# Kernel optimization log

Hardware: AMD Instinct MI355X
Metric: run time of the kernel (lower is better)

Reference implementation:

```python
import jax, jax.numpy as jnp
import numpy as np

MINIMUM_VALUE = -1e9  # C.MINIMUM_VALUE: large negative fill for masked positions


def setup_inputs() -> dict:
    key = jax.random.key(0)
    kq, kv, km, kw = jax.random.split(key, 4)
    B, N, H = 8, 2048, 1024
    query = jax.random.normal(kq, (B, N, H), dtype=jnp.float32)
    value = jax.random.normal(kv, (B, N, H), dtype=jnp.float32)
    mask = jax.random.randint(km, (B, N, N), 0, 2, dtype=jnp.int32)
    W = jax.random.normal(kw, (H, H), dtype=jnp.float32)
    return {"query": query, "value": value, "mask": mask, "W": W}


def reference(query, value, mask, W):
    # intermediate = query @ W           : B x M x H
    # e = relu(intermediate @ value^T)   : B x M x N
    e = jax.nn.relu(jnp.einsum("bmh,hk,bnk->bmn", query, W, value))
    attn_logits = jnp.where(mask > 0, e, MINIMUM_VALUE)
    attn = jax.nn.softmax(attn_logits, axis=-1)
    output = jnp.einsum("bmn,bnh->bmh", attn, value)
    return (output, attn)
```

## Files before the change

### kernel.cpp

```cpp
#include <hip/hip_runtime.h>


typedef _Float16 half8 __attribute__((ext_vector_type(8)));
typedef float f32x4 __attribute__((ext_vector_type(4)));
typedef unsigned short u16;
typedef unsigned int u32;

#define BATCH 8
#define SEQ   2048
#define HID   1024
#define MINV  (-1e9f)

#define AS1 __attribute__((address_space(1)))
#define AS3 __attribute__((address_space(3)))

__device__ __forceinline__ u16 h2u(_Float16 h) { return __builtin_bit_cast(u16, h); }

__device__ __forceinline__ u32 packhl(float x) {
    _Float16 h = (_Float16)x;
    _Float16 l = (_Float16)(x - (float)h);
    return (u32)h2u(h) | ((u32)h2u(l) << 16);
}

__device__ __forceinline__ void gload16(const char* g, AS3 char* l) {
    __builtin_amdgcn_global_load_lds((const AS1 void*)g, (AS3 void*)l, 16, 0, 0);
}

__global__ __launch_bounds__(256) void prep_v(const float* __restrict__ V,
                                              u16* __restrict__ Vp,
                                              u16* __restrict__ Vt)
{
    __shared__ __align__(16) u16 lt[64 * 72];
    const int b = blockIdx.z, n0 = blockIdx.y * 64, h0 = blockIdx.x * 64;
    const int t = threadIdx.x;
    const int r = t >> 4, c4 = (t & 15) * 4;
#pragma unroll
    for (int it = 0; it < 4; ++it) {
        const int rr = r + it * 16;
        const float4 x = *(const float4*)(V + ((size_t)b * SEQ + n0 + rr) * HID + h0 + c4);
        const float xs[4] = {x.x, x.y, x.z, x.w};
        u32 p[4];
#pragma unroll
        for (int e = 0; e < 4; ++e) {
            p[e] = packhl(xs[e]);
            lt[(c4 + e) * 72 + rr] = (u16)p[e];
        }
        const int g = (h0 + c4) >> 5, j = c4 & 31;
        u16* base = Vp + (((size_t)b * SEQ + n0 + rr) * 32 + g) * 64;
        *(uint2*)(base + j) = make_uint2((p[0] & 0xffffu) | (p[1] << 16),
                                         (p[2] & 0xffffu) | (p[3] << 16));
        *(uint2*)(base + 32 + j) = make_uint2((p[0] >> 16) | (p[1] & 0xffff0000u),
                                              (p[2] >> 16) | (p[3] & 0xffff0000u));
    }
    __syncthreads();
    const int hr = t >> 2, cc = (t & 3) * 2;
    uint4 v0 = *(const uint4*)&lt[hr * 72 + cc * 8];
    uint4 v1 = *(const uint4*)&lt[hr * 72 + cc * 8 + 8];
    u16* dst = Vt + ((size_t)b * HID + h0 + hr) * SEQ + n0 + cc * 8;
    *(uint4*)dst = v0;
    *(uint4*)(dst + 8) = v1;
}

__global__ __launch_bounds__(256) void prep_w(const float* __restrict__ W,
                                              u16* __restrict__ Wtp)
{
    __shared__ __align__(16) u32 lt[64 * 68];
    const int n0 = blockIdx.x * 64, k0 = blockIdx.y * 64;
    const int t = threadIdx.x;
    const int r = t >> 4, c4 = (t & 15) * 4;
#pragma unroll
    for (int it = 0; it < 4; ++it) {
        const int rr = r + it * 16;
        const float4 x = *(const float4*)(W + (size_t)(k0 + rr) * HID + n0 + c4);
        const float xs[4] = {x.x, x.y, x.z, x.w};
#pragma unroll
        for (int e = 0; e < 4; ++e) lt[(c4 + e) * 68 + rr] = packhl(xs[e]);
    }
    __syncthreads();
    const int n = t >> 2;
#pragma unroll
    for (int s = 0; s < 4; ++s) {
        const int ci = (t & 3) + s * 4;
        uint4 v = *(const uint4*)&lt[n * 68 + ci * 4];
        const int k = k0 + ci * 4;
        u16* base = Wtp + (((size_t)n0 + n) * 32 + (k >> 5)) * 64;
        const int j = k & 31;
        *(uint2*)(base + j) = make_uint2((v.x & 0xffffu) | (v.y << 16),
                                         (v.z & 0xffffu) | (v.w << 16));
        *(uint2*)(base + 32 + j) = make_uint2((v.x >> 16) | (v.y & 0xffff0000u),
                                              (v.z >> 16) | (v.w & 0xffff0000u));
    }
}

__global__ __launch_bounds__(256) void prep_q(const float* __restrict__ Q,
                                              u16* __restrict__ Qp)
{
    const size_t row = blockIdx.x;
    const int t = threadIdx.x;
    const float4 x = ((const float4*)(Q + row * HID))[t];
    const u32 p0 = packhl(x.x), p1 = packhl(x.y), p2 = packhl(x.z), p3 = packhl(x.w);
    const int k = t * 4;
    u16* base = Qp + (row * 32 + (k >> 5)) * 64;
    const int j = k & 31;
    *(uint2*)(base + j) = make_uint2((p0 & 0xffffu) | (p1 << 16),
                                     (p2 & 0xffffu) | (p3 << 16));
    *(uint2*)(base + 32 + j) = make_uint2((p0 >> 16) | (p1 & 0xffff0000u),
                                          (p2 >> 16) | (p3 & 0xffff0000u));
}

template <bool SPLIT>
__device__ __forceinline__ void cluster4x2(f32x4 (&acc)[8][4], int ib, int jb,
                                           const half8 (&ah)[4], const half8 (&al)[4],
                                           half8 bh0, half8 bl0, half8 bh1, half8 bl1)
{
#pragma unroll
    for (int f = 0; f < 4; ++f) {
#pragma unroll
        for (int jj = 0; jj < 2; ++jj) {
            const half8 bh = jj ? bh1 : bh0;
            const half8 bl = jj ? bl1 : bl0;
            f32x4 c = acc[ib + f][jb + jj];
            if constexpr (SPLIT) {
                c = __builtin_amdgcn_mfma_f32_16x16x32_f16(al[f], bh, c, 0, 0, 0);
                c = __builtin_amdgcn_mfma_f32_16x16x32_f16(ah[f], bl, c, 0, 0, 0);
                c = __builtin_amdgcn_mfma_f32_16x16x32_f16(ah[f], bh, c, 0, 0, 0);
            } else {
                c = __builtin_amdgcn_mfma_f32_16x16x32_f16(ah[f], bh, c, 0, 0, 0);
                c = __builtin_amdgcn_mfma_f32_16x16x32_f16(al[f], bl, c, 0, 0, 0);
            }
            acc[ib + f][jb + jj] = c;
        }
    }
}

template <int MODE>
__global__ __launch_bounds__(512, 2) void gemm_mfma(
    const char* __restrict__ Abase, const char* __restrict__ Bbase,
    void* __restrict__ Cbase, const int* __restrict__ Mbase,
    int ldc, long sAb, long sBb, long sC, long sM)
{
    constexpr bool SPLIT = (MODE != 3);
    extern __shared__ __align__(16) char smem[];

    const int nx = gridDim.x, ny = gridDim.y;
    const int nxy = nx * ny;
    int wg = blockIdx.x + nx * (blockIdx.y + ny * blockIdx.z);
    const int cpx = (nxy * gridDim.z) >> 3;
    wg = (wg & 7) * cpx + (wg >> 3);
    const int bz = wg / nxy;
    const int rem = wg - bz * nxy;
    const int m0 = (rem / nx) * 256, n0 = (rem % nx) * 256;

    const int tid = threadIdx.x;
    const int w = tid >> 6, l = tid & 63;
    const int wm = w >> 2, wn = w & 3;
    const int lm = l & 15, q = l >> 4;

    const char* Ab = Abase + (long)bz * sAb;
    const char* Bb = Bbase + (long)bz * sBb;

    u32 aoffs[4], boffs[4];
    int dsto[4];
#pragma unroll
    for (int it = 0; it < 4; ++it) {
        const int off = it * 8192 + tid * 16;
        dsto[it] = off;
        const int row = off >> 7;
        const int swi = (off & 127) ^ ((row & 7) << 4);
        aoffs[it] = (u32)(m0 + row) * 4096u + (u32)swi;
        boffs[it] = (u32)(n0 + row) * 4096u + (u32)swi;
    }
    const int wofs = (q * 16) ^ ((lm & 7) << 4);

    f32x4 acc[8][4];
#pragma unroll
    for (int i = 0; i < 8; ++i)
#pragma unroll
        for (int j = 0; j < 4; ++j) acc[i][j] = (f32x4){0.f, 0.f, 0.f, 0.f};

    AS3 char* lds = (AS3 char*)smem;

#pragma unroll
    for (int it = 0; it < 4; ++it) gload16(Ab + aoffs[it], lds + dsto[it]);
#pragma unroll
    for (int it = 0; it < 4; ++it) gload16(Bb + boffs[it], lds + 32768 + dsto[it]);
    asm volatile("s_waitcnt vmcnt(0)" ::: "memory");
    __builtin_amdgcn_s_barrier();

    half8 ah[4], al[4];
    half8 b0h, b0l, b1h, b1l, b2h, b2l, b3h, b3l;

    for (int ks = 0; ks < 32; ++ks) {
        const int cur = ks & 1;
        const char* At = smem + cur * 65536;
        const char* Bt = At + 32768;
        AS3 char* ldsA = lds + (cur ^ 1) * 65536;
        AS3 char* ldsB = ldsA + 32768;
        const u32 kb = (u32)(ks + 1) * 128u;
        const bool more = (ks < 31);

#pragma unroll
        for (int i = 0; i < 4; ++i) {
            const char* rp = At + ((i >> 1) * 64 + wm * 32 + (i & 1) * 16 + lm) * 128;
            ah[i] = *(const half8*)(rp + wofs);
            al[i] = *(const half8*)(rp + (wofs ^ 64));
        }
        {
            const char* cp0 = Bt + (wn * 32 + lm) * 128;
            b0h = *(const half8*)(cp0 + wofs);
            b0l = *(const half8*)(cp0 + (wofs ^ 64));
            const char* cp1 = Bt + (wn * 32 + 16 + lm) * 128;
            b1h = *(const half8*)(cp1 + wofs);
            b1l = *(const half8*)(cp1 + (wofs ^ 64));
            const char* cp2 = Bt + (128 + wn * 32 + lm) * 128;
            b2h = *(const half8*)(cp2 + wofs);
            b2l = *(const half8*)(cp2 + (wofs ^ 64));
            const char* cp3 = Bt + (128 + wn * 32 + 16 + lm) * 128;
            b3h = *(const half8*)(cp3 + wofs);
            b3l = *(const half8*)(cp3 + (wofs ^ 64));
        }
        if (more) {
#pragma unroll
            for (int it = 0; it < 4; ++it) gload16(Ab + (aoffs[it] + kb), ldsA + dsto[it]);
#pragma unroll
            for (int it = 0; it < 4; ++it) gload16(Bb + (boffs[it] + kb), ldsB + dsto[it]);
        }

        asm volatile("s_waitcnt lgkmcnt(4)" ::: "memory");
        __builtin_amdgcn_sched_barrier(0);
        __builtin_amdgcn_s_setprio(1);
        cluster4x2<SPLIT>(acc, 0, 0, ah, al, b0h, b0l, b1h, b1l);
        __builtin_amdgcn_s_setprio(0);

        asm volatile("s_waitcnt lgkmcnt(0)" ::: "memory");
        __builtin_amdgcn_sched_barrier(0);
        __builtin_amdgcn_s_setprio(1);
        cluster4x2<SPLIT>(acc, 0, 2, ah, al, b2h, b2l, b3h, b3l);
        __builtin_amdgcn_s_setprio(0);

#pragma unroll
        for (int i = 0; i < 4; ++i) {
            const char* rp = At + (128 + (i >> 1) * 64 + wm * 32 + (i & 1) * 16 + lm) * 128;
            ah[i] = *(const half8*)(rp + wofs);
            al[i] = *(const half8*)(rp + (wofs ^ 64));
        }
        asm volatile("s_waitcnt lgkmcnt(0)" ::: "memory");
        __builtin_amdgcn_sched_barrier(0);
        __builtin_amdgcn_s_setprio(1);
        cluster4x2<SPLIT>(acc, 4, 2, ah, al, b2h, b2l, b3h, b3l);
        cluster4x2<SPLIT>(acc, 4, 0, ah, al, b0h, b0l, b1h, b1l);
        __builtin_amdgcn_s_setprio(0);
        __builtin_amdgcn_sched_barrier(0);

        asm volatile("s_waitcnt vmcnt(0)" ::: "memory");
        __builtin_amdgcn_s_barrier();
    }

#pragma unroll
    for (int i = 0; i < 8; ++i) {
        const int arow = (i >> 1) * 64 + wm * 32 + (i & 1) * 16 + q * 4;
#pragma unroll
        for (int r = 0; r < 4; ++r) {
            const int grow = m0 + arow + r;
#pragma unroll
            for (int j = 0; j < 4; ++j) {
                const int gcol = n0 + (j >> 1) * 128 + wn * 32 + (j & 1) * 16 + lm;
                const float v = acc[i][j][r];
                if constexpr (MODE == 1) {
                    const u32 p = packhl(v);
                    u16* base = (u16*)Cbase + ((size_t)grow * (ldc >> 5) + (gcol >> 5)) * 64;
                    base[gcol & 31] = (u16)p;
                    base[32 + (gcol & 31)] = (u16)(p >> 16);
                } else if constexpr (MODE == 2) {
                    const int mv = Mbase[(long)bz * sM + (long)grow * ldc + gcol];
                    ((float*)Cbase)[(long)bz * sC + (long)grow * ldc + gcol] =
                        (mv > 0) ? fmaxf(v, 0.f) : MINV;
                } else {
                    ((float*)Cbase)[(long)bz * sC + (long)grow * ldc + gcol] = v;
                }
            }
        }
    }
}

__global__ __launch_bounds__(256) void softmax2048(float* __restrict__ attn,
                                                   u16* __restrict__ attnH)
{
    const long row = blockIdx.x;
    float* p = attn + row * 2048;
    const int tid = threadIdx.x;

    float4 v0 = ((const float4*)p)[tid];
    float4 v1 = ((const float4*)p)[tid + 256];

    float mx = fmaxf(fmaxf(fmaxf(v0.x, v0.y), fmaxf(v0.z, v0.w)),
                     fmaxf(fmaxf(v1.x, v1.y), fmaxf(v1.z, v1.w)));
#pragma unroll
    for (int o = 32; o >= 1; o >>= 1)
        mx = fmaxf(mx, __shfl_xor(mx, o, 64));

    __shared__ float redm[4];
    __shared__ float reds[4];
    const int wid = tid >> 6, lane = tid & 63;
    if (lane == 0) redm[wid] = mx;
    __syncthreads();
    mx = fmaxf(fmaxf(redm[0], redm[1]), fmaxf(redm[2], redm[3]));

    float e[8];
    e[0] = __expf(v0.x - mx); e[1] = __expf(v0.y - mx);
    e[2] = __expf(v0.z - mx); e[3] = __expf(v0.w - mx);
    e[4] = __expf(v1.x - mx); e[5] = __expf(v1.y - mx);
    e[6] = __expf(v1.z - mx); e[7] = __expf(v1.w - mx);

    float s = ((e[0] + e[1]) + (e[2] + e[3])) + ((e[4] + e[5]) + (e[6] + e[7]));
#pragma unroll
    for (int o = 32; o >= 1; o >>= 1)
        s += __shfl_xor(s, o, 64);
    if (lane == 0) reds[wid] = s;
    __syncthreads();
    s = (reds[0] + reds[1]) + (reds[2] + reds[3]);

    const float inv = 1.0f / s;
    float o0 = e[0] * inv, o1 = e[1] * inv, o2 = e[2] * inv, o3 = e[3] * inv;
    float o4 = e[4] * inv, o5 = e[5] * inv, o6 = e[6] * inv, o7 = e[7] * inv;
    ((float4*)p)[tid]       = make_float4(o0, o1, o2, o3);
    ((float4*)p)[tid + 256] = make_float4(o4, o5, o6, o7);

    u16* ph = attnH + row * 2048;
    ((uint2*)ph)[tid] =
        make_uint2((u32)h2u((_Float16)o0) | ((u32)h2u((_Float16)o1) << 16),
                   (u32)h2u((_Float16)o2) | ((u32)h2u((_Float16)o3) << 16));
    ((uint2*)ph)[tid + 256] =
        make_uint2((u32)h2u((_Float16)o4) | ((u32)h2u((_Float16)o5) << 16),
                   (u32)h2u((_Float16)o6) | ((u32)h2u((_Float16)o7) << 16));
}

extern "C" void kernel_launch(void* const* d_in, const int* in_sizes, int n_in,
                              void* d_out, int out_size, void* d_ws, size_t ws_size,
                              hipStream_t stream)
{
    (void)in_sizes; (void)n_in; (void)out_size; (void)ws_size;

    const float* query = (const float*)d_in[0];
    const float* value = (const float*)d_in[1];
    const int*   mask  = (const int*)d_in[2];
    const float* W     = (const float*)d_in[3];

    float* out  = (float*)d_out;
    float* attn = out + (size_t)BATCH * SEQ * HID;

    u16* Vp  = (u16*)d_ws;
    u16* Vt  = (u16*)((char*)d_ws + ((size_t)64 << 20));
    u16* Wtp = (u16*)((char*)d_ws + ((size_t)96 << 20));

    u16* interP = (u16*)d_out;
    u16* Qp     = (u16*)attn;
    u16* attnH  = Vp;

    static int attr_done = 0;
    if (!attr_done) {
        hipFuncSetAttribute((const void*)gemm_mfma<1>,
                            hipFuncAttributeMaxDynamicSharedMemorySize, 131072);
        hipFuncSetAttribute((const void*)gemm_mfma<2>,
                            hipFuncAttributeMaxDynamicSharedMemorySize, 131072);
        hipFuncSetAttribute((const void*)gemm_mfma<3>,
                            hipFuncAttributeMaxDynamicSharedMemorySize, 131072);
        attr_done = 1;
    }

    prep_v<<<dim3(HID / 64, SEQ / 64, BATCH), 256, 0, stream>>>(value, Vp, Vt);
    prep_w<<<dim3(HID / 64, HID / 64, 1), 256, 0, stream>>>(W, Wtp);
    prep_q<<<dim3(BATCH * SEQ), 256, 0, stream>>>(query, Qp);

    gemm_mfma<1><<<dim3(HID / 256, (BATCH * SEQ) / 256, 1), 512, 131072, stream>>>(
        (const char*)Qp, (const char*)Wtp, interP, nullptr,
        HID, 0, 0, 0, 0);

    gemm_mfma<2><<<dim3(SEQ / 256, SEQ / 256, BATCH), 512, 131072, stream>>>(
        (const char*)interP, (const char*)Vp, attn, mask,
        SEQ, (long)SEQ * 4096, (long)SEQ * 4096, (long)SEQ * SEQ, (long)SEQ * SEQ);

    softmax2048<<<dim3(BATCH * SEQ), 256, 0, stream>>>(attn, attnH);

    gemm_mfma<3><<<dim3(HID / 256, SEQ / 256, BATCH), 512, 131072, stream>>>(
        (const char*)attnH, (const char*)Vt, out, nullptr,
        HID, (long)SEQ * 4096, (long)HID * 4096, (long)SEQ * HID, 0);
}
```

Measured before the change: 728.8 us.

## Software-pipeline MFMA clusters across k-steps and prefetch mask bits during GEMM

```diff
diff --git a/kernel.cpp b/kernel.cpp
--- a/kernel.cpp
+++ b/kernel.cpp
@@ -5,6 +5,7 @@
 typedef float f32x4 __attribute__((ext_vector_type(4)));
 typedef unsigned short u16;
 typedef unsigned int u32;
+typedef unsigned long long u64;
 
 #define BATCH 8
 #define SEQ   2048
@@ -133,6 +134,8 @@
     }
 }
 
+#define SBAR() __builtin_amdgcn_sched_barrier(0)
+
 template <int MODE>
 __global__ __launch_bounds__(512, 2) void gemm_mfma(
     const char* __restrict__ Abase, const char* __restrict__ Bbase,
@@ -158,6 +161,7 @@
 
     const char* Ab = Abase + (long)bz * sAb;
     const char* Bb = Bbase + (long)bz * sBb;
+    const int* Mb = Mbase + (long)bz * sM;
 
     u32 aoffs[4], boffs[4];
     int dsto[4];
@@ -184,11 +188,11 @@
     for (int it = 0; it < 4; ++it) gload16(Ab + aoffs[it], lds + dsto[it]);
 #pragma unroll
     for (int it = 0; it < 4; ++it) gload16(Bb + boffs[it], lds + 32768 + dsto[it]);
-    asm volatile("s_waitcnt vmcnt(0)" ::: "memory");
-    __builtin_amdgcn_s_barrier();
-
-    half8 ah[4], al[4];
+
+    half8 ah0[4], al0[4], ah1[4], al1[4];
     half8 b0h, b0l, b1h, b1l, b2h, b2l, b3h, b3l;
+    int mtmp[8];
+    u64 mlo = 0, mhi = 0;
 
     for (int ks = 0; ks < 32; ++ks) {
         const int cur = ks & 1;
@@ -197,13 +201,16 @@
         AS3 char* ldsA = lds + (cur ^ 1) * 65536;
         AS3 char* ldsB = ldsA + 32768;
         const u32 kb = (u32)(ks + 1) * 128u;
-        const bool more = (ks < 31);
+
+        asm volatile("s_waitcnt vmcnt(0)" ::: "memory");
+        __builtin_amdgcn_s_barrier();
+        SBAR();
 
 #pragma unroll
         for (int i = 0; i < 4; ++i) {
             const char* rp = At + ((i >> 1) * 64 + wm * 32 + (i & 1) * 16 + lm) * 128;
-            ah[i] = *(const half8*)(rp + wofs);
-            al[i] = *(const half8*)(rp + (wofs ^ 64));
+            ah0[i] = *(const half8*)(rp + wofs);
+            al0[i] = *(const half8*)(rp + (wofs ^ 64));
         }
         {
             const char* cp0 = Bt + (wn * 32 + lm) * 128;
@@ -212,6 +219,42 @@
             const char* cp1 = Bt + (wn * 32 + 16 + lm) * 128;
             b1h = *(const half8*)(cp1 + wofs);
             b1l = *(const half8*)(cp1 + (wofs ^ 64));
+        }
+        if (ks < 31) {
+#pragma unroll
+            for (int it = 0; it < 4; ++it) gload16(Ab + (aoffs[it] + kb), ldsA + dsto[it]);
+#pragma unroll
+            for (int it = 0; it < 4; ++it) gload16(Bb + (boffs[it] + kb), ldsB + dsto[it]);
+        }
+        if constexpr (MODE == 2) {
+            const int s = ks - 16;
+            if (s >= 0) {
+                if (s > 0) {
+                    u32 m = 0;
+#pragma unroll
+                    for (int e = 0; e < 8; ++e) m |= (mtmp[e] > 0 ? 1u : 0u) << e;
+                    const int p = s - 1;
+                    if (p < 8) mlo |= (u64)m << (p * 8);
+                    else       mhi |= (u64)m << ((p - 8) * 8);
+                }
+                const int i_ = s >> 1, rb = (s & 1) * 2;
+                const long growb = (long)(m0 + (i_ >> 1) * 64 + wm * 32 + (i_ & 1) * 16 + q * 4);
+#pragma unroll
+                for (int e = 0; e < 8; ++e) {
+                    const int r = rb + (e >> 2), jj = e & 3;
+                    const int gcol = n0 + (jj >> 1) * 128 + wn * 32 + (jj & 1) * 16 + lm;
+                    mtmp[e] = Mb[(growb + r) * ldc + gcol];
+                }
+            }
+        }
+        SBAR();
+        if (ks > 0) {
+            __builtin_amdgcn_s_setprio(1);
+            cluster4x2<SPLIT>(acc, 4, 2, ah1, al1, b2h, b2l, b3h, b3l);
+            __builtin_amdgcn_s_setprio(0);
+        }
+        SBAR();
+        {
             const char* cp2 = Bt + (128 + wn * 32 + lm) * 128;
             b2h = *(const half8*)(cp2 + wofs);
             b2l = *(const half8*)(cp2 + (wofs ^ 64));
@@ -219,41 +262,35 @@
             b3h = *(const half8*)(cp3 + wofs);
             b3l = *(const half8*)(cp3 + (wofs ^ 64));
         }
-        if (more) {
-#pragma unroll
-            for (int it = 0; it < 4; ++it) gload16(Ab + (aoffs[it] + kb), ldsA + dsto[it]);
-#pragma unroll
-            for (int it = 0; it < 4; ++it) gload16(Bb + (boffs[it] + kb), ldsB + dsto[it]);
-        }
-
-        asm volatile("s_waitcnt lgkmcnt(4)" ::: "memory");
-        __builtin_amdgcn_sched_barrier(0);
+        SBAR();
         __builtin_amdgcn_s_setprio(1);
-        cluster4x2<SPLIT>(acc, 0, 0, ah, al, b0h, b0l, b1h, b1l);
+        cluster4x2<SPLIT>(acc, 0, 0, ah0, al0, b0h, b0l, b1h, b1l);
         __builtin_amdgcn_s_setprio(0);
-
-        asm volatile("s_waitcnt lgkmcnt(0)" ::: "memory");
-        __builtin_amdgcn_sched_barrier(0);
-        __builtin_amdgcn_s_setprio(1);
-        cluster4x2<SPLIT>(acc, 0, 2, ah, al, b2h, b2l, b3h, b3l);
-        __builtin_amdgcn_s_setprio(0);
-
+        SBAR();
 #pragma unroll
         for (int i = 0; i < 4; ++i) {
             const char* rp = At + (128 + (i >> 1) * 64 + wm * 32 + (i & 1) * 16 + lm) * 128;
-            ah[i] = *(const half8*)(rp + wofs);
-            al[i] = *(const half8*)(rp + (wofs ^ 64));
-        }
-        asm volatile("s_waitcnt lgkmcnt(0)" ::: "memory");
-        __builtin_amdgcn_sched_barrier(0);
+            ah1[i] = *(const half8*)(rp + wofs);
+            al1[i] = *(const half8*)(rp + (wofs ^ 64));
+        }
+        SBAR();
         __builtin_amdgcn_s_setprio(1);
-        cluster4x2<SPLIT>(acc, 4, 2, ah, al, b2h, b2l, b3h, b3l);
-        cluster4x2<SPLIT>(acc, 4, 0, ah, al, b0h, b0l, b1h, b1l);
+        cluster4x2<SPLIT>(acc, 0, 2, ah0, al0, b2h, b2l, b3h, b3l);
         __builtin_amdgcn_s_setprio(0);
-        __builtin_amdgcn_sched_barrier(0);
-
-        asm volatile("s_waitcnt vmcnt(0)" ::: "memory");
-        __builtin_amdgcn_s_barrier();
+        SBAR();
+        __builtin_amdgcn_s_setprio(1);
+        cluster4x2<SPLIT>(acc, 4, 0, ah1, al1, b0h, b0l, b1h, b1l);
+        __builtin_amdgcn_s_setprio(0);
+    }
+
+    __builtin_amdgcn_s_setprio(1);
+    cluster4x2<SPLIT>(acc, 4, 2, ah1, al1, b2h, b2l, b3h, b3l);
+    __builtin_amdgcn_s_setprio(0);
+    if constexpr (MODE == 2) {
+        u32 m = 0;
+#pragma unroll
+        for (int e = 0; e < 8; ++e) m |= (mtmp[e] > 0 ? 1u : 0u) << e;
+        mhi |= (u64)m << 56;
     }
 
 #pragma unroll
@@ -272,9 +309,12 @@
                     base[gcol & 31] = (u16)p;
                     base[32 + (gcol & 31)] = (u16)(p >> 16);
                 } else if constexpr (MODE == 2) {
-                    const int mv = Mbase[(long)bz * sM + (long)grow * ldc + gcol];
+                    const int s = i * 2 + (r >> 1);
+                    const int bp = (r & 1) * 4 + j;
+                    const u32 bit = (s < 8) ? (u32)(mlo >> (s * 8 + bp)) & 1u
+                                            : (u32)(mhi >> ((s - 8) * 8 + bp)) & 1u;
                     ((float*)Cbase)[(long)bz * sC + (long)grow * ldc + gcol] =
-                        (mv > 0) ? fmaxf(v, 0.f) : MINV;
+                        bit ? fmaxf(v, 0.f) : MINV;
                 } else {
                     ((float*)Cbase)[(long)bz * sC + (long)grow * ldc + gcol] = v;
                 }
```

Measured after the change: 732.7 us. About the same (+0.5%).

## Shrink GEMM block tile to 128x128 with 4 waves and restructured pipeline

Applied to the files above, without the earlier changes.

```diff
diff --git a/kernel.cpp b/kernel.cpp
--- a/kernel.cpp
+++ b/kernel.cpp
@@ -109,32 +109,33 @@
 }
 
 template <bool SPLIT>
-__device__ __forceinline__ void cluster4x2(f32x4 (&acc)[8][4], int ib, int jb,
+__device__ __forceinline__ void cluster4x2(f32x4 (&acc)[4][4], int jb,
                                            const half8 (&ah)[4], const half8 (&al)[4],
-                                           half8 bh0, half8 bl0, half8 bh1, half8 bl1)
+                                           const half8 (&bh)[4], const half8 (&bl)[4])
 {
 #pragma unroll
     for (int f = 0; f < 4; ++f) {
 #pragma unroll
         for (int jj = 0; jj < 2; ++jj) {
-            const half8 bh = jj ? bh1 : bh0;
-            const half8 bl = jj ? bl1 : bl0;
-            f32x4 c = acc[ib + f][jb + jj];
+            const int j = jb + jj;
+            f32x4 c = acc[f][j];
             if constexpr (SPLIT) {
-                c = __builtin_amdgcn_mfma_f32_16x16x32_f16(al[f], bh, c, 0, 0, 0);
-                c = __builtin_amdgcn_mfma_f32_16x16x32_f16(ah[f], bl, c, 0, 0, 0);
-                c = __builtin_amdgcn_mfma_f32_16x16x32_f16(ah[f], bh, c, 0, 0, 0);
+                c = __builtin_amdgcn_mfma_f32_16x16x32_f16(al[f], bh[j], c, 0, 0, 0);
+                c = __builtin_amdgcn_mfma_f32_16x16x32_f16(ah[f], bl[j], c, 0, 0, 0);
+                c = __builtin_amdgcn_mfma_f32_16x16x32_f16(ah[f], bh[j], c, 0, 0, 0);
             } else {
-                c = __builtin_amdgcn_mfma_f32_16x16x32_f16(ah[f], bh, c, 0, 0, 0);
-                c = __builtin_amdgcn_mfma_f32_16x16x32_f16(al[f], bl, c, 0, 0, 0);
+                c = __builtin_amdgcn_mfma_f32_16x16x32_f16(ah[f], bh[j], c, 0, 0, 0);
+                c = __builtin_amdgcn_mfma_f32_16x16x32_f16(al[f], bl[j], c, 0, 0, 0);
             }
-            acc[ib + f][jb + jj] = c;
+            acc[f][j] = c;
         }
     }
 }
 
+#define SBAR() __builtin_amdgcn_sched_barrier(0)
+
 template <int MODE>
-__global__ __launch_bounds__(512, 2) void gemm_mfma(
+__global__ __launch_bounds__(256, 2) void gemm_mfma(
     const char* __restrict__ Abase, const char* __restrict__ Bbase,
     void* __restrict__ Cbase, const int* __restrict__ Mbase,
     int ldc, long sAb, long sBb, long sC, long sM)
@@ -149,11 +150,11 @@
     wg = (wg & 7) * cpx + (wg >> 3);
     const int bz = wg / nxy;
     const int rem = wg - bz * nxy;
-    const int m0 = (rem / nx) * 256, n0 = (rem % nx) * 256;
+    const int m0 = (rem / nx) * 128, n0 = (rem % nx) * 128;
 
     const int tid = threadIdx.x;
     const int w = tid >> 6, l = tid & 63;
-    const int wm = w >> 2, wn = w & 3;
+    const int wm = w >> 1, wn = w & 1;
     const int lm = l & 15, q = l >> 4;
 
     const char* Ab = Abase + (long)bz * sAb;
@@ -163,7 +164,7 @@
     int dsto[4];
 #pragma unroll
     for (int it = 0; it < 4; ++it) {
-        const int off = it * 8192 + tid * 16;
+        const int off = it * 4096 + tid * 16;
         dsto[it] = off;
         const int row = off >> 7;
         const int swi = (off & 127) ^ ((row & 7) << 4);
@@ -172,9 +173,9 @@
     }
     const int wofs = (q * 16) ^ ((lm & 7) << 4);
 
-    f32x4 acc[8][4];
-#pragma unroll
-    for (int i = 0; i < 8; ++i)
+    f32x4 acc[4][4];
+#pragma unroll
+    for (int i = 0; i < 4; ++i)
 #pragma unroll
         for (int j = 0; j < 4; ++j) acc[i][j] = (f32x4){0.f, 0.f, 0.f, 0.f};
 
@@ -183,88 +184,71 @@
 #pragma unroll
     for (int it = 0; it < 4; ++it) gload16(Ab + aoffs[it], lds + dsto[it]);
 #pragma unroll
-    for (int it = 0; it < 4; ++it) gload16(Bb + boffs[it], lds + 32768 + dsto[it]);
-    asm volatile("s_waitcnt vmcnt(0)" ::: "memory");
-    __builtin_amdgcn_s_barrier();
-
-    half8 ah[4], al[4];
-    half8 b0h, b0l, b1h, b1l, b2h, b2l, b3h, b3l;
+    for (int it = 0; it < 4; ++it) gload16(Bb + boffs[it], lds + 16384 + dsto[it]);
+
+    half8 ah[4], al[4], bh[4], bl[4];
 
     for (int ks = 0; ks < 32; ++ks) {
         const int cur = ks & 1;
-        const char* At = smem + cur * 65536;
-        const char* Bt = At + 32768;
-        AS3 char* ldsA = lds + (cur ^ 1) * 65536;
-        AS3 char* ldsB = ldsA + 32768;
+        const char* At = smem + cur * 32768;
+        const char* Bt = At + 16384;
+        AS3 char* ldsA = lds + (cur ^ 1) * 32768;
+        AS3 char* ldsB = ldsA + 16384;
         const u32 kb = (u32)(ks + 1) * 128u;
-        const bool more = (ks < 31);
-
-#pragma unroll
-        for (int i = 0; i < 4; ++i) {
-            const char* rp = At + ((i >> 1) * 64 + wm * 32 + (i & 1) * 16 + lm) * 128;
-            ah[i] = *(const half8*)(rp + wofs);
-            al[i] = *(const half8*)(rp + (wofs ^ 64));
-        }
-        {
-            const char* cp0 = Bt + (wn * 32 + lm) * 128;
-            b0h = *(const half8*)(cp0 + wofs);
-            b0l = *(const half8*)(cp0 + (wofs ^ 64));
-            const char* cp1 = Bt + (wn * 32 + 16 + lm) * 128;
-            b1h = *(const half8*)(cp1 + wofs);
-            b1l = *(const half8*)(cp1 + (wofs ^ 64));
-            const char* cp2 = Bt + (128 + wn * 32 + lm) * 128;
-            b2h = *(const half8*)(cp2 + wofs);
-            b2l = *(const half8*)(cp2 + (wofs ^ 64));
-            const char* cp3 = Bt + (128 + wn * 32 + 16 + lm) * 128;
-            b3h = *(const half8*)(cp3 + wofs);
-            b3l = *(const half8*)(cp3 + (wofs ^ 64));
-        }
-        if (more) {
-#pragma unroll
-            for (int it = 0; it < 4; ++it) gload16(Ab + (aoffs[it] + kb), ldsA + dsto[it]);
-#pragma unroll
-            for (int it = 0; it < 4; ++it) gload16(Bb + (boffs[it] + kb), ldsB + dsto[it]);
-        }
-
-        asm volatile("s_waitcnt lgkmcnt(4)" ::: "memory");
-        __builtin_amdgcn_sched_barrier(0);
-        __builtin_amdgcn_s_setprio(1);
-        cluster4x2<SPLIT>(acc, 0, 0, ah, al, b0h, b0l, b1h, b1l);
-        __builtin_amdgcn_s_setprio(0);
-
-        asm volatile("s_waitcnt lgkmcnt(0)" ::: "memory");
-        __builtin_amdgcn_sched_barrier(0);
-        __builtin_amdgcn_s_setprio(1);
-        cluster4x2<SPLIT>(acc, 0, 2, ah, al, b2h, b2l, b3h, b3l);
-        __builtin_amdgcn_s_setprio(0);
-
-#pragma unroll
-        for (int i = 0; i < 4; ++i) {
-            const char* rp = At + (128 + (i >> 1) * 64 + wm * 32 + (i & 1) * 16 + lm) * 128;
-            ah[i] = *(const half8*)(rp + wofs);
-            al[i] = *(const half8*)(rp + (wofs ^ 64));
-        }
-        asm volatile("s_waitcnt lgkmcnt(0)" ::: "memory");
-        __builtin_amdgcn_sched_barrier(0);
-        __builtin_amdgcn_s_setprio(1);
-        cluster4x2<SPLIT>(acc, 4, 2, ah, al, b2h, b2l, b3h, b3l);
-        cluster4x2<SPLIT>(acc, 4, 0, ah, al, b0h, b0l, b1h, b1l);
-        __builtin_amdgcn_s_setprio(0);
-        __builtin_amdgcn_sched_barrier(0);
 
         asm volatile("s_waitcnt vmcnt(0)" ::: "memory");
         __builtin_amdgcn_s_barrier();
-    }
-
-#pragma unroll
-    for (int i = 0; i < 8; ++i) {
-        const int arow = (i >> 1) * 64 + wm * 32 + (i & 1) * 16 + q * 4;
+        SBAR();
+
+        {
+            const char* arp = At + (wm * 64 + lm) * 128 + wofs;
+            const char* alp = At + (wm * 64 + lm) * 128 + (wofs ^ 64);
+#pragma unroll
+            for (int i = 0; i < 4; ++i) {
+                ah[i] = *(const half8*)(arp + i * 2048);
+                al[i] = *(const half8*)(alp + i * 2048);
+            }
+            const char* brp = Bt + (wn * 64 + lm) * 128 + wofs;
+            const char* blp = Bt + (wn * 64 + lm) * 128 + (wofs ^ 64);
+            bh[0] = *(const half8*)(brp);
+            bl[0] = *(const half8*)(blp);
+            bh[1] = *(const half8*)(brp + 2048);
+            bl[1] = *(const half8*)(blp + 2048);
+            if (ks < 31) {
+#pragma unroll
+                for (int it = 0; it < 4; ++it) gload16(Ab + (aoffs[it] + kb), ldsA + dsto[it]);
+#pragma unroll
+                for (int it = 0; it < 4; ++it) gload16(Bb + (boffs[it] + kb), ldsB + dsto[it]);
+            }
+            bh[2] = *(const half8*)(brp + 2 * 2048);
+            bl[2] = *(const half8*)(blp + 2 * 2048);
+            bh[3] = *(const half8*)(brp + 3 * 2048);
+            bl[3] = *(const half8*)(blp + 3 * 2048);
+        }
+
+        asm volatile("s_waitcnt lgkmcnt(4)" ::: "memory");
+        SBAR();
+        __builtin_amdgcn_s_setprio(1);
+        cluster4x2<SPLIT>(acc, 0, ah, al, bh, bl);
+        __builtin_amdgcn_s_setprio(0);
+
+        asm volatile("s_waitcnt lgkmcnt(0)" ::: "memory");
+        SBAR();
+        __builtin_amdgcn_s_setprio(1);
+        cluster4x2<SPLIT>(acc, 2, ah, al, bh, bl);
+        __builtin_amdgcn_s_setprio(0);
+        SBAR();
+    }
+
+#pragma unroll
+    for (int i = 0; i < 4; ++i) {
+        const int arow = wm * 64 + i * 16 + q * 4;
 #pragma unroll
         for (int r = 0; r < 4; ++r) {
             const int grow = m0 + arow + r;
 #pragma unroll
             for (int j = 0; j < 4; ++j) {
-                const int gcol = n0 + (j >> 1) * 128 + wn * 32 + (j & 1) * 16 + lm;
+                const int gcol = n0 + wn * 64 + j * 16 + lm;
                 const float v = acc[i][j][r];
                 if constexpr (MODE == 1) {
                     const u32 p = packhl(v);
@@ -360,11 +344,11 @@
     static int attr_done = 0;
     if (!attr_done) {
         hipFuncSetAttribute((const void*)gemm_mfma<1>,
-                            hipFuncAttributeMaxDynamicSharedMemorySize, 131072);
+                            hipFuncAttributeMaxDynamicSharedMemorySize, 65536);
         hipFuncSetAttribute((const void*)gemm_mfma<2>,
-                            hipFuncAttributeMaxDynamicSharedMemorySize, 131072);
+                            hipFuncAttributeMaxDynamicSharedMemorySize, 65536);
         hipFuncSetAttribute((const void*)gemm_mfma<3>,
-                            hipFuncAttributeMaxDynamicSharedMemorySize, 131072);
+                            hipFuncAttributeMaxDynamicSharedMemorySize, 65536);
         attr_done = 1;
     }
 
@@ -372,17 +356,17 @@
     prep_w<<<dim3(HID / 64, HID / 64, 1), 256, 0, stream>>>(W, Wtp);
     prep_q<<<dim3(BATCH * SEQ), 256, 0, stream>>>(query, Qp);
 
-    gemm_mfma<1><<<dim3(HID / 256, (BATCH * SEQ) / 256, 1), 512, 131072, stream>>>(
+    gemm_mfma<1><<<dim3(HID / 128, (BATCH * SEQ) / 128, 1), 256, 65536, stream>>>(
         (const char*)Qp, (const char*)Wtp, interP, nullptr,
         HID, 0, 0, 0, 0);
 
-    gemm_mfma<2><<<dim3(SEQ / 256, SEQ / 256, BATCH), 512, 131072, stream>>>(
+    gemm_mfma<2><<<dim3(SEQ / 128, SEQ / 128, BATCH), 256, 65536, stream>>>(
         (const char*)interP, (const char*)Vp, attn, mask,
         SEQ, (long)SEQ * 4096, (long)SEQ * 4096, (long)SEQ * SEQ, (long)SEQ * SEQ);
 
     softmax2048<<<dim3(BATCH * SEQ), 256, 0, stream>>>(attn, attnH);
 
-    gemm_mfma<3><<<dim3(HID / 256, SEQ / 256, BATCH), 512, 131072, stream>>>(
+    gemm_mfma<3><<<dim3(HID / 128, SEQ / 128, BATCH), 256, 65536, stream>>>(
         (const char*)attnH, (const char*)Vt, out, nullptr,
         HID, (long)SEQ * 4096, (long)HID * 4096, (long)SEQ * HID, 0);
 }
```

Result: slower. 747.9 us (+2.6%).

## Rotate LDS read order per wave half and unroll k-loop by two buffers

Applied to the files above, without the earlier changes.

```diff
diff --git a/kernel.cpp b/kernel.cpp
--- a/kernel.cpp
+++ b/kernel.cpp
@@ -133,15 +133,114 @@
     }
 }
 
+#define SBAR() __builtin_amdgcn_sched_barrier(0)
+
+template <int MODE, int ROT, int CUR>
+__device__ __forceinline__ void kstep(
+    const char* pAh, const char* pAl, const char* pBh, const char* pBl,
+    AS3 char* lds,
+    const char* __restrict__ Ab, const char* __restrict__ Bb,
+    const u32 (&aoffs)[4], const u32 (&boffs)[4], const int (&dsto)[4],
+    u32 kb, bool more, f32x4 (&acc)[8][4])
+{
+    constexpr bool SPLIT = (MODE != 3);
+    constexpr int FH = (ROT == 0) ? 0 : 16384;
+    constexpr int SH = 16384 - FH;
+    constexpr int GF = (ROT == 0) ? 0 : 16384;
+    constexpr int GS = 16384 - GF;
+    constexpr int AQ1 = (ROT == 0) ? 0 : 4;
+    constexpr int AQ2 = 4 - AQ1;
+    constexpr int BQ1 = (ROT == 0) ? 0 : 2;
+    constexpr int BQ2 = 2 - BQ1;
+    AS3 char* ldsA = lds + (CUR ^ 1) * 65536;
+    AS3 char* ldsB = ldsA + 32768;
+
+    asm volatile("s_waitcnt vmcnt(0)" ::: "memory");
+    __builtin_amdgcn_s_barrier();
+    SBAR();
+
+    half8 ah[4], al[4];
+#pragma unroll
+    for (int i = 0; i < 4; ++i) {
+        const int off = FH + (i >> 1) * 8192 + (i & 1) * 2048;
+        ah[i] = *(const half8*)(pAh + off);
+        al[i] = *(const half8*)(pAl + off);
+    }
+    half8 bFh0 = *(const half8*)(pBh + GF);
+    half8 bFl0 = *(const half8*)(pBl + GF);
+    half8 bFh1 = *(const half8*)(pBh + GF + 2048);
+    half8 bFl1 = *(const half8*)(pBl + GF + 2048);
+    if (more) {
+#pragma unroll
+        for (int it = 0; it < 4; ++it) gload16(Ab + (aoffs[it] + kb), ldsA + dsto[it]);
+#pragma unroll
+        for (int it = 0; it < 4; ++it) gload16(Bb + (boffs[it] + kb), ldsB + dsto[it]);
+    }
+    half8 bSh0 = *(const half8*)(pBh + GS);
+    half8 bSl0 = *(const half8*)(pBl + GS);
+    half8 bSh1 = *(const half8*)(pBh + GS + 2048);
+    half8 bSl1 = *(const half8*)(pBl + GS + 2048);
+
+    asm volatile("s_waitcnt lgkmcnt(4)" ::: "memory");
+    SBAR();
+    __builtin_amdgcn_s_setprio(1);
+    cluster4x2<SPLIT>(acc, AQ1, BQ1, ah, al, bFh0, bFl0, bFh1, bFl1);
+    __builtin_amdgcn_s_setprio(0);
+
+    asm volatile("s_waitcnt lgkmcnt(0)" ::: "memory");
+    SBAR();
+    __builtin_amdgcn_s_setprio(1);
+    cluster4x2<SPLIT>(acc, AQ1, BQ2, ah, al, bSh0, bSl0, bSh1, bSl1);
+    __builtin_amdgcn_s_setprio(0);
+
+#pragma unroll
+    for (int i = 0; i < 4; ++i) {
+        const int off = SH + (i >> 1) * 8192 + (i & 1) * 2048;
+        ah[i] = *(const half8*)(pAh + off);
+        al[i] = *(const half8*)(pAl + off);
+    }
+    asm volatile("s_waitcnt lgkmcnt(0)" ::: "memory");
+    SBAR();
+    __builtin_amdgcn_s_setprio(1);
+    cluster4x2<SPLIT>(acc, AQ2, BQ2, ah, al, bSh0, bSl0, bSh1, bSl1);
+    cluster4x2<SPLIT>(acc, AQ2, BQ1, ah, al, bFh0, bFl0, bFh1, bFl1);
+    __builtin_amdgcn_s_setprio(0);
+    SBAR();
+}
+
+template <int MODE, int ROT>
+__device__ __forceinline__ void kloop(
+    char* smem, const char* __restrict__ Ab, const char* __restrict__ Bb,
+    const u32 (&aoffs)[4], const u32 (&boffs)[4], const int (&dsto)[4],
+    int baseAhi, int baseAlo, int baseBhi, int baseBlo, f32x4 (&acc)[8][4])
+{
+    AS3 char* lds = (AS3 char*)smem;
+    const char* pA0h = smem + baseAhi;
+    const char* pA0l = smem + baseAlo;
+    const char* pB0h = smem + baseBhi;
+    const char* pB0l = smem + baseBlo;
+    const char* pA1h = pA0h + 65536;
+    const char* pA1l = pA0l + 65536;
+    const char* pB1h = pB0h + 65536;
+    const char* pB1l = pB0l + 65536;
+
+    for (int ks = 0; ks < 32; ks += 2) {
+        const u32 kb0 = (u32)(ks + 1) * 128u;
+        const u32 kb1 = (u32)(ks + 2) * 128u;
+        kstep<MODE, ROT, 0>(pA0h, pA0l, pB0h, pB0l, lds, Ab, Bb,
+                            aoffs, boffs, dsto, kb0, true, acc);
+        kstep<MODE, ROT, 1>(pA1h, pA1l, pB1h, pB1l, lds, Ab, Bb,
+                            aoffs, boffs, dsto, kb1, ks < 30, acc);
+    }
+}
+
 template <int MODE>
-__global__ __launch_bounds__(512, 2) void gemm_mfma(
+__device__ __forceinline__ void gemm_body(
+    char* smem,
     const char* __restrict__ Abase, const char* __restrict__ Bbase,
     void* __restrict__ Cbase, const int* __restrict__ Mbase,
     int ldc, long sAb, long sBb, long sC, long sM)
 {
-    constexpr bool SPLIT = (MODE != 3);
-    extern __shared__ __align__(16) char smem[];
-
     const int nx = gridDim.x, ny = gridDim.y;
     const int nxy = nx * ny;
     int wg = blockIdx.x + nx * (blockIdx.y + ny * blockIdx.z);
@@ -171,6 +270,10 @@
         boffs[it] = (u32)(n0 + row) * 4096u + (u32)swi;
     }
     const int wofs = (q * 16) ^ ((lm & 7) << 4);
+    const int baseAhi = (wm * 32 + lm) * 128 + wofs;
+    const int baseAlo = (wm * 32 + lm) * 128 + (wofs ^ 64);
+    const int baseBhi = 32768 + (wn * 32 + lm) * 128 + wofs;
+    const int baseBlo = 32768 + (wn * 32 + lm) * 128 + (wofs ^ 64);
 
     f32x4 acc[8][4];
 #pragma unroll
@@ -184,77 +287,13 @@
     for (int it = 0; it < 4; ++it) gload16(Ab + aoffs[it], lds + dsto[it]);
 #pragma unroll
     for (int it = 0; it < 4; ++it) gload16(Bb + boffs[it], lds + 32768 + dsto[it]);
-    asm volatile("s_waitcnt vmcnt(0)" ::: "memory");
-    __builtin_amdgcn_s_barrier();
-
-    half8 ah[4], al[4];
-    half8 b0h, b0l, b1h, b1l, b2h, b2l, b3h, b3l;
-
-    for (int ks = 0; ks < 32; ++ks) {
-        const int cur = ks & 1;
-        const char* At = smem + cur * 65536;
-        const char* Bt = At + 32768;
-        AS3 char* ldsA = lds + (cur ^ 1) * 65536;
-        AS3 char* ldsB = ldsA + 32768;
-        const u32 kb = (u32)(ks + 1) * 128u;
-        const bool more = (ks < 31);
-
-#pragma unroll
-        for (int i = 0; i < 4; ++i) {
-            const char* rp = At + ((i >> 1) * 64 + wm * 32 + (i & 1) * 16 + lm) * 128;
-            ah[i] = *(const half8*)(rp + wofs);
-            al[i] = *(const half8*)(rp + (wofs ^ 64));
-        }
-        {
-            const char* cp0 = Bt + (wn * 32 + lm) * 128;
-            b0h = *(const half8*)(cp0 + wofs);
-            b0l = *(const half8*)(cp0 + (wofs ^ 64));
-            const char* cp1 = Bt + (wn * 32 + 16 + lm) * 128;
-            b1h = *(const half8*)(cp1 + wofs);
-            b1l = *(const half8*)(cp1 + (wofs ^ 64));
-            const char* cp2 = Bt + (128 + wn * 32 + lm) * 128;
-            b2h = *(const half8*)(cp2 + wofs);
-            b2l = *(const half8*)(cp2 + (wofs ^ 64));
-            const char* cp3 = Bt + (128 + wn * 32 + 16 + lm) * 128;
-            b3h = *(const half8*)(cp3 + wofs);
-            b3l = *(const half8*)(cp3 + (wofs ^ 64));
-        }
-        if (more) {
-#pragma unroll
-            for (int it = 0; it < 4; ++it) gload16(Ab + (aoffs[it] + kb), ldsA + dsto[it]);
-#pragma unroll
-            for (int it = 0; it < 4; ++it) gload16(Bb + (boffs[it] + kb), ldsB + dsto[it]);
-        }
-
-        asm volatile("s_waitcnt lgkmcnt(4)" ::: "memory");
-        __builtin_amdgcn_sched_barrier(0);
-        __builtin_amdgcn_s_setprio(1);
-        cluster4x2<SPLIT>(acc, 0, 0, ah, al, b0h, b0l, b1h, b1l);
-        __builtin_amdgcn_s_setprio(0);
-
-        asm volatile("s_waitcnt lgkmcnt(0)" ::: "memory");
-        __builtin_amdgcn_sched_barrier(0);
-        __builtin_amdgcn_s_setprio(1);
-        cluster4x2<SPLIT>(acc, 0, 2, ah, al, b2h, b2l, b3h, b3l);
-        __builtin_amdgcn_s_setprio(0);
-
-#pragma unroll
-        for (int i = 0; i < 4; ++i) {
-            const char* rp = At + (128 + (i >> 1) * 64 + wm * 32 + (i & 1) * 16 + lm) * 128;
-            ah[i] = *(const half8*)(rp + wofs);
-            al[i] = *(const half8*)(rp + (wofs ^ 64));
-        }
-        asm volatile("s_waitcnt lgkmcnt(0)" ::: "memory");
-        __builtin_amdgcn_sched_barrier(0);
-        __builtin_amdgcn_s_setprio(1);
-        cluster4x2<SPLIT>(acc, 4, 2, ah, al, b2h, b2l, b3h, b3l);
-        cluster4x2<SPLIT>(acc, 4, 0, ah, al, b0h, b0l, b1h, b1l);
-        __builtin_amdgcn_s_setprio(0);
-        __builtin_amdgcn_sched_barrier(0);
-
-        asm volatile("s_waitcnt vmcnt(0)" ::: "memory");
-        __builtin_amdgcn_s_barrier();
-    }
+
+    if (((w >> 2) & 1) == 0)
+        kloop<MODE, 0>(smem, Ab, Bb, aoffs, boffs, dsto,
+                       baseAhi, baseAlo, baseBhi, baseBlo, acc);
+    else
+        kloop<MODE, 1>(smem, Ab, Bb, aoffs, boffs, dsto,
+                       baseAhi, baseAlo, baseBhi, baseBlo, acc);
 
 #pragma unroll
     for (int i = 0; i < 8; ++i) {
@@ -283,6 +322,28 @@
     }
 }
 
+__global__ __launch_bounds__(512, 2) void gemm1_qw(
+    const char* __restrict__ A, const char* __restrict__ B, void* __restrict__ C,
+    const int* __restrict__ M, int ldc, long sAb, long sBb, long sC, long sM)
+{
+    extern __shared__ __align__(16) char smem[];
+    gemm_body<1>(smem, A, B, C, M, ldc, sAb, sBb, sC, sM);
+}
+__global__ __launch_bounds__(512, 2) void gemm2_av(
+    const char* __restrict__ A, const char* __restrict__ B, void* __restrict__ C,
+    const int* __restrict__ M, int ldc, long sAb, long sBb, long sC, long sM)
+{
+    extern __shared__ __align__(16) char smem[];
+    gemm_body<2>(smem, A, B, C, M, ldc, sAb, sBb, sC, sM);
+}
+__global__ __launch_bounds__(512, 2) void gemm3_out(
+    const char* __restrict__ A, const char* __restrict__ B, void* __restrict__ C,
+    const int* __restrict__ M, int ldc, long sAb, long sBb, long sC, long sM)
+{
+    extern __shared__ __align__(16) char smem[];
+    gemm_body<3>(smem, A, B, C, M, ldc, sAb, sBb, sC, sM);
+}
+
 __global__ __launch_bounds__(256) void softmax2048(float* __restrict__ attn,
                                                    u16* __restrict__ attnH)
 {
@@ -359,11 +420,11 @@
 
     static int attr_done = 0;
     if (!attr_done) {
-        hipFuncSetAttribute((const void*)gemm_mfma<1>,
+        hipFuncSetAttribute((const void*)gemm1_qw,
                             hipFuncAttributeMaxDynamicSharedMemorySize, 131072);
-        hipFuncSetAttribute((const void*)gemm_mfma<2>,
+        hipFuncSetAttribute((const void*)gemm2_av,
                             hipFuncAttributeMaxDynamicSharedMemorySize, 131072);
-        hipFuncSetAttribute((const void*)gemm_mfma<3>,
+        hipFuncSetAttribute((const void*)gemm3_out,
                             hipFuncAttributeMaxDynamicSharedMemorySize, 131072);
         attr_done = 1;
     }
@@ -372,17 +433,17 @@
     prep_w<<<dim3(HID / 64, HID / 64, 1), 256, 0, stream>>>(W, Wtp);
     prep_q<<<dim3(BATCH * SEQ), 256, 0, stream>>>(query, Qp);
 
-    gemm_mfma<1><<<dim3(HID / 256, (BATCH * SEQ) / 256, 1), 512, 131072, stream>>>(
+    gemm1_qw<<<dim3(HID / 256, (BATCH * SEQ) / 256, 1), 512, 131072, stream>>>(
         (const char*)Qp, (const char*)Wtp, interP, nullptr,
         HID, 0, 0, 0, 0);
 
-    gemm_mfma<2><<<dim3(SEQ / 256, SEQ / 256, BATCH), 512, 131072, stream>>>(
+    gemm2_av<<<dim3(SEQ / 256, SEQ / 256, BATCH), 512, 131072, stream>>>(
         (const char*)interP, (const char*)Vp, attn, mask,
         SEQ, (long)SEQ * 4096, (long)SEQ * 4096, (long)SEQ * SEQ, (long)SEQ * SEQ);
 
     softmax2048<<<dim3(BATCH * SEQ), 256, 0, stream>>>(attn, attnH);
 
-    gemm_mfma<3><<<dim3(HID / 256, SEQ / 256, BATCH), 512, 131072, stream>>>(
+    gemm3_out<<<dim3(HID / 256, SEQ / 256, BATCH), 512, 131072, stream>>>(
         (const char*)attnH, (const char*)Vt, out, nullptr,
         HID, (long)SEQ * 4096, (long)HID * 4096, (long)SEQ * HID, 0);
 }
```

Result: no change. 715.9 us (-1.8%).
